# Optimization experiments

Hardware: AMD Instinct MI355X
Metric: run time of the kernel (lower is better)

## Reference

```python
import jax, jax.numpy as jnp
import numpy as np

B, H, L, TAU, THETA = 8192, 256, 4, 8, 8


def setup_inputs() -> dict:
    key = jax.random.key(0)
    ks = jax.random.split(key, 16)
    w = lambda k, shape: (jax.random.normal(k, shape, jnp.float32) * 0.02)
    return {
        "x": jax.random.normal(ks[0], (B, H), jnp.float32),
        "t_att": jax.random.normal(ks[1], (L, TAU, B, H), jnp.float32),
        "s_att": jax.random.normal(ks[2], (L, TAU, B, H), jnp.float32),
        "embed_w": w(ks[3], (H, H)),
        "embed_b": jnp.zeros((H,), jnp.float32),
        "wtn": w(ks[4], (L, H, H)),
        "btn": jnp.zeros((L, H), jnp.float32),
        "wsn": w(ks[5], (L, H, H)),
        "bsn": jnp.zeros((L, H), jnp.float32),
        "wt": w(ks[6], (L, 3 * H, H)),
        "bt": jnp.zeros((L, 3 * H), jnp.float32),
        "ws": w(ks[7], (L, 3 * H, H)),
        "bs": jnp.zeros((L, 3 * H), jnp.float32),
        "out_w": w(ks[8], (H, H)),
        "out_b": jnp.zeros((H,), jnp.float32),
    }


def _forward(x, t_att, s_att, embed_w, embed_b, wtn, btn, wsn, bsn, wt, bt, ws, bs, out_w, out_b):
    n_layers, tau = t_att.shape[0], t_att.shape[1]
    b, h = x.shape
    scale = 1.0 / np.sqrt(h).astype(np.float32)
    theta = THETA

    S = x @ embed_w.T + embed_b  # embed: [B, H]
    # rolling spatial buffers, start as theta zero entries
    t_sp = jnp.zeros((theta, b, h), x.dtype)
    s_sp = jnp.zeros((theta, b, h), x.dtype)

    for i in range(n_layers):
        T_last = t_att[i, -1]  # [B, H]
        # append current S_t / last T_t to spatial buffers, keep last theta
        s_sp = jnp.concatenate([s_sp[1:], S[None]], axis=0)
        t_sp = jnp.concatenate([t_sp[1:], T_last[None]], axis=0)
        # s_att[i].append(S_t); slice last tau -> keys include current S
        s_keys = jnp.concatenate([s_att[i, 1:], S[None]], axis=0)  # [tau, B, H]
        t_vals = t_att[i]  # [tau, B, H]

        s_next = S @ wsn[i].T + bsn[i]
        t_next = T_last @ wtn[i].T + btn[i]

        # temporal attention over last-tau history
        w_t = jax.nn.softmax(jnp.einsum('kbh,bh->kb', s_keys, s_next) * scale, axis=0)
        T_trend = jnp.einsum('kb,kbh->bh', w_t, t_vals)
        t_gate = jax.nn.sigmoid(t_next)
        T_fusion = T_last * t_gate + (1.0 - t_gate) * T_trend

        # spatial attention over last-theta buffer
        w_s = jax.nn.softmax(jnp.einsum('kbh,bh->kb', t_sp, t_next) * scale, axis=0)
        S_trend = jnp.einsum('kb,kbh->bh', w_s, s_sp)
        s_gate = jax.nn.sigmoid(s_next)
        S_fusion = S * s_gate + (1.0 - s_gate) * S_trend

        Tc = T_fusion @ wt[i].T + bt[i]  # [B, 3H]
        Sc = S_fusion @ ws[i].T + bs[i]
        t_g, t_t_, t_s_ = jnp.split(Tc, 3, axis=-1)
        s_g, s_t_, s_s_ = jnp.split(Sc, 3, axis=-1)
        Tg = jax.nn.sigmoid(t_g)
        Sg = jax.nn.sigmoid(s_g)
        # T_new feeds the (stateful) history; S carries to next layer
        S = Sg * s_s_ + (1.0 - Sg) * t_s_

    return jnp.tanh(S @ out_w.T + out_b)


def reference(x, t_att, s_att, embed_w, embed_b, wtn, btn, wsn, bsn, wt, bt, ws, bs, out_w, out_b):
    return _forward(x, t_att, s_att, embed_w, embed_b, wtn, btn, wsn, bsn, wt, bt, ws, bs, out_w, out_b)
```

## Files before the change

kernel.cpp:

```cpp
#include <hip/hip_runtime.h>
#include <cmath>

typedef __attribute__((ext_vector_type(8))) short short8;
typedef __attribute__((ext_vector_type(4))) float f32x4;
typedef __attribute__((ext_vector_type(4))) unsigned short us4;
typedef unsigned short u16;

#define BATCH 8192
#define HDIM  256
static constexpr size_t BH = (size_t)BATCH * HDIM;
#define PAD 264

__device__ __forceinline__ u16 f2bf(float f) {
    union { float f; unsigned u; } v; v.f = f;
    unsigned r = v.u + 0x7FFFu + ((v.u >> 16) & 1u);
    return (u16)(r >> 16);
}
__device__ __forceinline__ float bf2f(u16 u) {
    union { unsigned u; float f; } v; v.u = ((unsigned)u) << 16;
    return v.f;
}
__device__ __forceinline__ float sigmoidf_(float x) {
    return 1.f / (1.f + __expf(-x));
}
__device__ __forceinline__ short8 cvt8(const float* p) {
    f32x4 lo = *(const f32x4*)p, hi = *(const f32x4*)(p + 4);
    short8 t;
    t[0] = (short)f2bf(lo[0]); t[1] = (short)f2bf(lo[1]);
    t[2] = (short)f2bf(lo[2]); t[3] = (short)f2bf(lo[3]);
    t[4] = (short)f2bf(hi[0]); t[5] = (short)f2bf(hi[1]);
    t[6] = (short)f2bf(hi[2]); t[7] = (short)f2bf(hi[3]);
    return t;
}
__device__ __forceinline__ float dot4(const f32x4& a, const float* b) {
    return a[0] * b[0] + a[1] * b[1] + a[2] * b[2] + a[3] * b[3];
}
template<int N>
__device__ __forceinline__ void vmwait() {
    asm volatile("s_waitcnt vmcnt(%0)" :: "n"(N) : "memory");
    __builtin_amdgcn_sched_barrier(0);
}

__global__ __launch_bounds__(256) void convert_weights(
    const float* __restrict__ embed_w, const float* __restrict__ wtn,
    const float* __restrict__ wsn, const float* __restrict__ wt,
    const float* __restrict__ ws, const float* __restrict__ out_w,
    u16* __restrict__ dst)
{
    int idx = blockIdx.x * 256 + threadIdx.x;
    int e = idx * 4;
    if (e >= 22 * 65536) return;
    int c = e >> 16, o = e & 65535;
    const float* src;
    if (c == 0)      src = embed_w + o;
    else if (c < 5)  src = wtn + (size_t)(c - 1) * 65536 + o;
    else if (c < 9)  src = wsn + (size_t)(c - 5) * 65536 + o;
    else if (c < 13) src = wt + (size_t)(c - 9) * 768 * 256 + 512 * 256 + o;
    else if (c < 17) src = ws + (size_t)(c - 13) * 768 * 256 + o;
    else if (c < 21) src = ws + (size_t)(c - 17) * 768 * 256 + 512 * 256 + o;
    else             src = out_w + o;
    f32x4 v = *(const f32x4*)src;
    us4 r;
#pragma unroll
    for (int j = 0; j < 4; ++j) r[j] = f2bf(v[j]);
    *(us4*)(dst + e) = r;
}

template<int I>
__device__ __forceinline__ void issue_row(f32x4 (&buf)[18],
    const float* __restrict__ t_att, const float* __restrict__ s_att,
    int row, int lane)
{
    const size_t ro = (size_t)row * 256 + lane * 4;
    const float* sa = s_att + (size_t)I * 8 * BH + ro;
    const float* ta = t_att + (size_t)I * 8 * BH + ro;
#pragma unroll
    for (int kk = 0; kk < 7; ++kk)
        asm volatile("global_load_dwordx4 %0, %1, off"
                     : "=v"(buf[kk]) : "v"(sa + (size_t)(kk + 1) * BH));
#pragma unroll
    for (int kk = 0; kk < 8; ++kk)
        asm volatile("global_load_dwordx4 %0, %1, off"
                     : "=v"(buf[7 + kk]) : "v"(ta + (size_t)kk * BH));
#pragma unroll
    for (int jj = 0; jj < I; ++jj)
        asm volatile("global_load_dwordx4 %0, %1, off"
                     : "=v"(buf[15 + jj]) : "v"(t_att + ((size_t)jj * 8 + 7) * BH + ro));
}

template<int I>
__device__ __forceinline__ void compute_row(
    const f32x4 (&buf)[18], int rr, int lane,
    u16 (&S_lds)[5][16][PAD], u16 (&sn_lds)[16][PAD], u16 (&tn_lds)[16][PAD],
    u16 (&tf_lds)[16][PAD], u16 (&sf_lds)[16][PAD])
{
    const float scale = 0.0625f;
    us4 snu = *(const us4*)&sn_lds[rr][lane * 4];
    us4 tnu = *(const us4*)&tn_lds[rr][lane * 4];
    us4 scu = *(const us4*)&S_lds[I][rr][lane * 4];
    float sn[4], tn[4], Sc[4];
#pragma unroll
    for (int j = 0; j < 4; ++j) { sn[j] = bf2f(snu[j]); tn[j] = bf2f(tnu[j]); Sc[j] = bf2f(scu[j]); }

    constexpr int NV = 9 + I;
    float v[NV];
#pragma unroll
    for (int kk = 0; kk < 7; ++kk) v[kk] = dot4(buf[kk], sn);
    v[7] = Sc[0] * sn[0] + Sc[1] * sn[1] + Sc[2] * sn[2] + Sc[3] * sn[3];
#pragma unroll
    for (int jj = 0; jj < I; ++jj) v[8 + jj] = dot4(buf[15 + jj], tn);
    v[8 + I] = dot4(buf[14], tn);

#pragma unroll
    for (int o = 32; o > 0; o >>= 1)
#pragma unroll
        for (int u = 0; u < NV; ++u) v[u] += __shfl_xor(v[u], o);

    float m = v[0] * scale;
#pragma unroll
    for (int kk = 1; kk < 8; ++kk) m = fmaxf(m, v[kk] * scale);
    float w8[8], den = 0.f;
#pragma unroll
    for (int kk = 0; kk < 8; ++kk) { w8[kk] = __expf(v[kk] * scale - m); den += w8[kk]; }
    float inv = 1.f / den;

    float Tt[4] = {0.f, 0.f, 0.f, 0.f};
#pragma unroll
    for (int kk = 0; kk < 8; ++kk)
#pragma unroll
        for (int j = 0; j < 4; ++j) Tt[j] += w8[kk] * buf[7 + kk][j];
    us4 ot;
#pragma unroll
    for (int j = 0; j < 4; ++j) {
        float g = sigmoidf_(tn[j]);
        ot[j] = f2bf(buf[14][j] * g + (1.f - g) * Tt[j] * inv);
    }
    *(us4*)&tf_lds[rr][lane * 4] = ot;

    float ms = fmaxf(0.f, v[8 + I] * scale);
#pragma unroll
    for (int jj = 0; jj < I; ++jj) ms = fmaxf(ms, v[8 + jj] * scale);
    float dens = (float)(7 - I) * __expf(-ms);
    float St[4];
    {
        float w = __expf(v[8 + I] * scale - ms);
        dens += w;
#pragma unroll
        for (int j = 0; j < 4; ++j) St[j] = w * Sc[j];
    }
#pragma unroll
    for (int jj = 0; jj < I; ++jj) {
        float w = __expf(v[8 + jj] * scale - ms);
        dens += w;
        us4 shu = *(const us4*)&S_lds[jj][rr][lane * 4];
#pragma unroll
        for (int j = 0; j < 4; ++j) St[j] += w * bf2f(shu[j]);
    }
    float invs = 1.f / dens;
    us4 os;
#pragma unroll
    for (int j = 0; j < 4; ++j) {
        float g = sigmoidf_(sn[j]);
        os[j] = f2bf(Sc[j] * g + (1.f - g) * St[j] * invs);
    }
    *(us4*)&sf_lds[rr][lane * 4] = os;
}

template<int I>
__device__ __forceinline__ void layer_body(
    const float* __restrict__ t_att, const float* __restrict__ s_att,
    const u16* __restrict__ Wbf,
    const float* __restrict__ btn, const float* __restrict__ bsn,
    const float* __restrict__ bt, const float* __restrict__ bs,
    u16 (&S_lds)[5][16][PAD], u16 (&sn_lds)[16][PAD], u16 (&tn_lds)[16][PAD],
    u16 (&tf_lds)[16][PAD], u16 (&sf_lds)[16][PAD],
    int lane, int wave, int lr, int kg, int row0)
{
    {
        const int g = wave >> 1;
        const int n0 = (wave & 1) * 128;
        const u16* Wm = Wbf + (size_t)((g ? 1 : 5) + I) * 65536;
        const float* bias = (g ? btn : bsn) + I * 256;
        f32x4 acc[8] = {};
        for (int k0 = 0; k0 < 256; k0 += 32) {
            int k = k0 + kg * 8;
            short8 a;
            if (g == 0) a = *(const short8*)(&S_lds[I][lr][k]);
            else        a = cvt8(t_att + ((size_t)I * 8 + 7) * BH + (size_t)(row0 + lr) * 256 + k);
#pragma unroll
            for (int nf = 0; nf < 8; ++nf) {
                short8 b = *(const short8*)(Wm + (size_t)(n0 + nf * 16 + lr) * 256 + k);
                acc[nf] = __builtin_amdgcn_mfma_f32_16x16x32_bf16(a, b, acc[nf], 0, 0, 0);
            }
        }
        u16 (*dst)[PAD] = g ? tn_lds : sn_lds;
#pragma unroll
        for (int nf = 0; nf < 8; ++nf) {
            int n = n0 + nf * 16 + lr;
            float bn = bias[n];
#pragma unroll
            for (int r = 0; r < 4; ++r)
                dst[kg * 4 + r][n] = f2bf(acc[nf][r] + bn);
        }
    }
    __syncthreads();

    {
        constexpr int NL = 15 + I;
        const int r0 = wave * 4;
        f32x4 A[18], B[18];
        issue_row<I>(A, t_att, s_att, row0 + r0, lane);
        issue_row<I>(B, t_att, s_att, row0 + r0 + 1, lane);
        vmwait<NL>();
        compute_row<I>(A, r0, lane, S_lds, sn_lds, tn_lds, tf_lds, sf_lds);
        issue_row<I>(A, t_att, s_att, row0 + r0 + 2, lane);
        vmwait<NL>();
        compute_row<I>(B, r0 + 1, lane, S_lds, sn_lds, tn_lds, tf_lds, sf_lds);
        issue_row<I>(B, t_att, s_att, row0 + r0 + 3, lane);
        vmwait<NL>();
        compute_row<I>(A, r0 + 2, lane, S_lds, sn_lds, tn_lds, tf_lds, sf_lds);
        vmwait<0>();
        compute_row<I>(B, r0 + 3, lane, S_lds, sn_lds, tn_lds, tf_lds, sf_lds);
    }
    __syncthreads();

    {
        const int n0 = wave * 64;
        const u16* Wt3 = Wbf + (size_t)(9  + I) * 65536;
        const u16* Ws1 = Wbf + (size_t)(13 + I) * 65536;
        const u16* Ws3 = Wbf + (size_t)(17 + I) * 65536;
        f32x4 aT[4] = {}, aG[4] = {}, aS[4] = {};
        for (int k0 = 0; k0 < 256; k0 += 32) {
            int k = k0 + kg * 8;
            short8 at = *(const short8*)(&tf_lds[lr][k]);
            short8 as = *(const short8*)(&sf_lds[lr][k]);
#pragma unroll
            for (int nf = 0; nf < 4; ++nf) {
                size_t wo = (size_t)(n0 + nf * 16 + lr) * 256 + k;
                aT[nf] = __builtin_amdgcn_mfma_f32_16x16x32_bf16(at, *(const short8*)(Wt3 + wo), aT[nf], 0, 0, 0);
                aG[nf] = __builtin_amdgcn_mfma_f32_16x16x32_bf16(as, *(const short8*)(Ws1 + wo), aG[nf], 0, 0, 0);
                aS[nf] = __builtin_amdgcn_mfma_f32_16x16x32_bf16(as, *(const short8*)(Ws3 + wo), aS[nf], 0, 0, 0);
            }
        }
        const float* b1 = bt + I * 768 + 512;
        const float* b2 = bs + I * 768;
        const float* b3 = bs + I * 768 + 512;
#pragma unroll
        for (int nf = 0; nf < 4; ++nf) {
            int n = n0 + nf * 16 + lr;
            float bb1 = b1[n], bb2 = b2[n], bb3 = b3[n];
#pragma unroll
            for (int r = 0; r < 4; ++r) {
                float gv = sigmoidf_(aG[nf][r] + bb2);
                float vv = gv * (aS[nf][r] + bb3) + (1.f - gv) * (aT[nf][r] + bb1);
                S_lds[I + 1][kg * 4 + r][n] = f2bf(vv);
            }
        }
    }
    __syncthreads();
}

__global__ __launch_bounds__(256, 2) void stau_mega(
    const float* __restrict__ x,
    const float* __restrict__ t_att, const float* __restrict__ s_att,
    const u16* __restrict__ Wbf,
    const float* __restrict__ embed_b,
    const float* __restrict__ btn, const float* __restrict__ bsn,
    const float* __restrict__ bt, const float* __restrict__ bs,
    const float* __restrict__ out_b,
    float* __restrict__ outp)
{
    __shared__ __align__(16) u16 S_lds[5][16][PAD];
    __shared__ __align__(16) u16 sn_lds[16][PAD];
    __shared__ __align__(16) u16 tn_lds[16][PAD];
    __shared__ __align__(16) u16 tf_lds[16][PAD];
    __shared__ __align__(16) u16 sf_lds[16][PAD];

    const int lane = threadIdx.x & 63;
    const int wave = threadIdx.x >> 6;
    const int lr = lane & 15;
    const int kg = lane >> 4;
    const int row0 = blockIdx.x * 16;

    {
        const int n0 = wave * 64;
        f32x4 acc[4] = {};
        for (int k0 = 0; k0 < 256; k0 += 32) {
            int k = k0 + kg * 8;
            short8 a = cvt8(x + (size_t)(row0 + lr) * 256 + k);
#pragma unroll
            for (int nf = 0; nf < 4; ++nf) {
                short8 b = *(const short8*)(Wbf + (size_t)(n0 + nf * 16 + lr) * 256 + k);
                acc[nf] = __builtin_amdgcn_mfma_f32_16x16x32_bf16(a, b, acc[nf], 0, 0, 0);
            }
        }
#pragma unroll
        for (int nf = 0; nf < 4; ++nf) {
            int n = n0 + nf * 16 + lr;
            float bn = embed_b[n];
#pragma unroll
            for (int r = 0; r < 4; ++r)
                S_lds[0][kg * 4 + r][n] = f2bf(acc[nf][r] + bn);
        }
    }
    __syncthreads();

    layer_body<0>(t_att, s_att, Wbf, btn, bsn, bt, bs,
                  S_lds, sn_lds, tn_lds, tf_lds, sf_lds, lane, wave, lr, kg, row0);
    layer_body<1>(t_att, s_att, Wbf, btn, bsn, bt, bs,
                  S_lds, sn_lds, tn_lds, tf_lds, sf_lds, lane, wave, lr, kg, row0);
    layer_body<2>(t_att, s_att, Wbf, btn, bsn, bt, bs,
                  S_lds, sn_lds, tn_lds, tf_lds, sf_lds, lane, wave, lr, kg, row0);
    layer_body<3>(t_att, s_att, Wbf, btn, bsn, bt, bs,
                  S_lds, sn_lds, tn_lds, tf_lds, sf_lds, lane, wave, lr, kg, row0);

    {
        const int n0 = wave * 64;
        const u16* Wo = Wbf + (size_t)21 * 65536;
        f32x4 acc[4] = {};
        for (int k0 = 0; k0 < 256; k0 += 32) {
            int k = k0 + kg * 8;
            short8 a = *(const short8*)(&S_lds[4][lr][k]);
#pragma unroll
            for (int nf = 0; nf < 4; ++nf) {
                short8 b = *(const short8*)(Wo + (size_t)(n0 + nf * 16 + lr) * 256 + k);
                acc[nf] = __builtin_amdgcn_mfma_f32_16x16x32_bf16(a, b, acc[nf], 0, 0, 0);
            }
        }
#pragma unroll
        for (int nf = 0; nf < 4; ++nf) {
            int n = n0 + nf * 16 + lr;
            float bn = out_b[n];
#pragma unroll
            for (int r = 0; r < 4; ++r)
                outp[(size_t)(row0 + kg * 4 + r) * 256 + n] = tanhf(acc[nf][r] + bn);
        }
    }
}

extern "C" void kernel_launch(void* const* d_in, const int* in_sizes, int n_in,
                              void* d_out, int out_size, void* d_ws, size_t ws_size,
                              hipStream_t stream)
{
    (void)in_sizes; (void)n_in; (void)out_size; (void)ws_size;
    const float* x       = (const float*)d_in[0];
    const float* t_att   = (const float*)d_in[1];
    const float* s_att   = (const float*)d_in[2];
    const float* embed_w = (const float*)d_in[3];
    const float* embed_b = (const float*)d_in[4];
    const float* wtn     = (const float*)d_in[5];
    const float* btn     = (const float*)d_in[6];
    const float* wsn     = (const float*)d_in[7];
    const float* bsn     = (const float*)d_in[8];
    const float* wt      = (const float*)d_in[9];
    const float* bt      = (const float*)d_in[10];
    const float* ws_in   = (const float*)d_in[11];
    const float* bs      = (const float*)d_in[12];
    const float* out_w   = (const float*)d_in[13];
    const float* out_b   = (const float*)d_in[14];

    u16* Wbf = (u16*)d_ws;

    convert_weights<<<1408, 256, 0, stream>>>(embed_w, wtn, wsn, wt, ws_in, out_w, Wbf);

    stau_mega<<<BATCH / 16, 256, 0, stream>>>(
        x, t_att, s_att, Wbf, embed_b, btn, bsn, bt, bs, out_b, (float*)d_out);
}
```

Before: 271.9 us.

## Move S history from LDS to global workspace and restructure per-row attention loads

```diff
diff --git a/kernel.cpp b/kernel.cpp
--- a/kernel.cpp
+++ b/kernel.cpp
@@ -9,7 +9,7 @@
 #define BATCH 8192
 #define HDIM  256
 static constexpr size_t BH = (size_t)BATCH * HDIM;
-#define PAD 264
+#define LPAD 264
 
 __device__ __forceinline__ u16 f2bf(float f) {
     union { float f; unsigned u; } v; v.f = f;
@@ -67,49 +67,65 @@
 }
 
 template<int I>
-__device__ __forceinline__ void issue_row(f32x4 (&buf)[18],
+__device__ __forceinline__ void attn_row(
     const float* __restrict__ t_att, const float* __restrict__ s_att,
-    int row, int lane)
-{
-    const size_t ro = (size_t)row * 256 + lane * 4;
+    const u16* __restrict__ S_hist,
+    int brow, int rr, int lane,
+    u16 (&sn_lds)[16][LPAD], u16 (&tn_lds)[16][LPAD],
+    u16 (&tf_lds)[16][LPAD], u16 (&sf_lds)[16][LPAD])
+{
+    const float scale = 0.0625f;
+    const size_t ro = (size_t)brow * 256 + lane * 4;
     const float* sa = s_att + (size_t)I * 8 * BH + ro;
     const float* ta = t_att + (size_t)I * 8 * BH + ro;
+
+    us4 scu;
+    us4 shu[I > 0 ? I : 1];
+    asm volatile("global_load_dwordx2 %0, %1, off"
+                 : "=v"(scu) : "v"(S_hist + (size_t)I * BH + ro));
+#pragma unroll
+    for (int jj = 0; jj < I; ++jj)
+        asm volatile("global_load_dwordx2 %0, %1, off"
+                     : "=v"(shu[jj]) : "v"(S_hist + (size_t)jj * BH + ro));
+
+    f32x4 dbuf[8 + I];
 #pragma unroll
     for (int kk = 0; kk < 7; ++kk)
         asm volatile("global_load_dwordx4 %0, %1, off"
-                     : "=v"(buf[kk]) : "v"(sa + (size_t)(kk + 1) * BH));
-#pragma unroll
-    for (int kk = 0; kk < 8; ++kk)
-        asm volatile("global_load_dwordx4 %0, %1, off"
-                     : "=v"(buf[7 + kk]) : "v"(ta + (size_t)kk * BH));
+                     : "=v"(dbuf[kk]) : "v"(sa + (size_t)(kk + 1) * BH));
 #pragma unroll
     for (int jj = 0; jj < I; ++jj)
         asm volatile("global_load_dwordx4 %0, %1, off"
-                     : "=v"(buf[15 + jj]) : "v"(t_att + ((size_t)jj * 8 + 7) * BH + ro));
-}
-
-template<int I>
-__device__ __forceinline__ void compute_row(
-    const f32x4 (&buf)[18], int rr, int lane,
-    u16 (&S_lds)[5][16][PAD], u16 (&sn_lds)[16][PAD], u16 (&tn_lds)[16][PAD],
-    u16 (&tf_lds)[16][PAD], u16 (&sf_lds)[16][PAD])
-{
-    const float scale = 0.0625f;
+                     : "=v"(dbuf[7 + jj]) : "v"(t_att + ((size_t)jj * 8 + 7) * BH + ro));
+    asm volatile("global_load_dwordx4 %0, %1, off"
+                 : "=v"(dbuf[7 + I]) : "v"(ta + (size_t)7 * BH));
+
+    f32x4 tbuf[7];
+#pragma unroll
+    for (int kk = 0; kk < 7; ++kk)
+        asm volatile("global_load_dwordx4 %0, %1, off"
+                     : "=v"(tbuf[kk]) : "v"(ta + (size_t)kk * BH));
+
     us4 snu = *(const us4*)&sn_lds[rr][lane * 4];
     us4 tnu = *(const us4*)&tn_lds[rr][lane * 4];
-    us4 scu = *(const us4*)&S_lds[I][rr][lane * 4];
-    float sn[4], tn[4], Sc[4];
-#pragma unroll
-    for (int j = 0; j < 4; ++j) { sn[j] = bf2f(snu[j]); tn[j] = bf2f(tnu[j]); Sc[j] = bf2f(scu[j]); }
+    float sn[4], tn[4];
+#pragma unroll
+    for (int j = 0; j < 4; ++j) { sn[j] = bf2f(snu[j]); tn[j] = bf2f(tnu[j]); }
+
+    vmwait<7>();
+
+    float Sc[4];
+#pragma unroll
+    for (int j = 0; j < 4; ++j) Sc[j] = bf2f(scu[j]);
 
     constexpr int NV = 9 + I;
     float v[NV];
 #pragma unroll
-    for (int kk = 0; kk < 7; ++kk) v[kk] = dot4(buf[kk], sn);
+    for (int kk = 0; kk < 7; ++kk) v[kk] = dot4(dbuf[kk], sn);
     v[7] = Sc[0] * sn[0] + Sc[1] * sn[1] + Sc[2] * sn[2] + Sc[3] * sn[3];
 #pragma unroll
-    for (int jj = 0; jj < I; ++jj) v[8 + jj] = dot4(buf[15 + jj], tn);
-    v[8 + I] = dot4(buf[14], tn);
+    for (int jj = 0; jj < I; ++jj) v[8 + jj] = dot4(dbuf[7 + jj], tn);
+    v[8 + I] = dot4(dbuf[7 + I], tn);
 
 #pragma unroll
     for (int o = 32; o > 0; o >>= 1)
@@ -124,16 +140,20 @@
     for (int kk = 0; kk < 8; ++kk) { w8[kk] = __expf(v[kk] * scale - m); den += w8[kk]; }
     float inv = 1.f / den;
 
-    float Tt[4] = {0.f, 0.f, 0.f, 0.f};
-#pragma unroll
-    for (int kk = 0; kk < 8; ++kk)
-#pragma unroll
-        for (int j = 0; j < 4; ++j) Tt[j] += w8[kk] * buf[7 + kk][j];
+    vmwait<0>();
+
+    float Tt[4];
+#pragma unroll
+    for (int j = 0; j < 4; ++j) Tt[j] = w8[7] * dbuf[7 + I][j];
+#pragma unroll
+    for (int kk = 0; kk < 7; ++kk)
+#pragma unroll
+        for (int j = 0; j < 4; ++j) Tt[j] += w8[kk] * tbuf[kk][j];
     us4 ot;
 #pragma unroll
     for (int j = 0; j < 4; ++j) {
         float g = sigmoidf_(tn[j]);
-        ot[j] = f2bf(buf[14][j] * g + (1.f - g) * Tt[j] * inv);
+        ot[j] = f2bf(dbuf[7 + I][j] * g + (1.f - g) * Tt[j] * inv);
     }
     *(us4*)&tf_lds[rr][lane * 4] = ot;
 
@@ -152,9 +172,8 @@
     for (int jj = 0; jj < I; ++jj) {
         float w = __expf(v[8 + jj] * scale - ms);
         dens += w;
-        us4 shu = *(const us4*)&S_lds[jj][rr][lane * 4];
-#pragma unroll
-        for (int j = 0; j < 4; ++j) St[j] += w * bf2f(shu[j]);
+#pragma unroll
+        for (int j = 0; j < 4; ++j) St[j] += w * bf2f(shu[jj][j]);
     }
     float invs = 1.f / dens;
     us4 os;
@@ -169,11 +188,11 @@
 template<int I>
 __device__ __forceinline__ void layer_body(
     const float* __restrict__ t_att, const float* __restrict__ s_att,
-    const u16* __restrict__ Wbf,
+    u16* __restrict__ S_hist, const u16* __restrict__ Wbf,
     const float* __restrict__ btn, const float* __restrict__ bsn,
     const float* __restrict__ bt, const float* __restrict__ bs,
-    u16 (&S_lds)[5][16][PAD], u16 (&sn_lds)[16][PAD], u16 (&tn_lds)[16][PAD],
-    u16 (&tf_lds)[16][PAD], u16 (&sf_lds)[16][PAD],
+    u16 (&sn_lds)[16][LPAD], u16 (&tn_lds)[16][LPAD],
+    u16 (&tf_lds)[16][LPAD], u16 (&sf_lds)[16][LPAD],
     int lane, int wave, int lr, int kg, int row0)
 {
     {
@@ -185,7 +204,7 @@
         for (int k0 = 0; k0 < 256; k0 += 32) {
             int k = k0 + kg * 8;
             short8 a;
-            if (g == 0) a = *(const short8*)(&S_lds[I][lr][k]);
+            if (g == 0) a = *(const short8*)(S_hist + (size_t)I * BH + (size_t)(row0 + lr) * 256 + k);
             else        a = cvt8(t_att + ((size_t)I * 8 + 7) * BH + (size_t)(row0 + lr) * 256 + k);
 #pragma unroll
             for (int nf = 0; nf < 8; ++nf) {
@@ -193,7 +212,7 @@
                 acc[nf] = __builtin_amdgcn_mfma_f32_16x16x32_bf16(a, b, acc[nf], 0, 0, 0);
             }
         }
-        u16 (*dst)[PAD] = g ? tn_lds : sn_lds;
+        u16 (*dst)[LPAD] = g ? tn_lds : sn_lds;
 #pragma unroll
         for (int nf = 0; nf < 8; ++nf) {
             int n = n0 + nf * 16 + lr;
@@ -205,22 +224,11 @@
     }
     __syncthreads();
 
-    {
-        constexpr int NL = 15 + I;
-        const int r0 = wave * 4;
-        f32x4 A[18], B[18];
-        issue_row<I>(A, t_att, s_att, row0 + r0, lane);
-        issue_row<I>(B, t_att, s_att, row0 + r0 + 1, lane);
-        vmwait<NL>();
-        compute_row<I>(A, r0, lane, S_lds, sn_lds, tn_lds, tf_lds, sf_lds);
-        issue_row<I>(A, t_att, s_att, row0 + r0 + 2, lane);
-        vmwait<NL>();
-        compute_row<I>(B, r0 + 1, lane, S_lds, sn_lds, tn_lds, tf_lds, sf_lds);
-        issue_row<I>(B, t_att, s_att, row0 + r0 + 3, lane);
-        vmwait<NL>();
-        compute_row<I>(A, r0 + 2, lane, S_lds, sn_lds, tn_lds, tf_lds, sf_lds);
-        vmwait<0>();
-        compute_row<I>(B, r0 + 3, lane, S_lds, sn_lds, tn_lds, tf_lds, sf_lds);
+#pragma unroll 1
+    for (int q = 0; q < 4; ++q) {
+        int rr = wave * 4 + q;
+        attn_row<I>(t_att, s_att, S_hist, row0 + rr, rr, lane,
+                    sn_lds, tn_lds, tf_lds, sf_lds);
     }
     __syncthreads();
 
@@ -242,6 +250,7 @@
                 aS[nf] = __builtin_amdgcn_mfma_f32_16x16x32_bf16(as, *(const short8*)(Ws3 + wo), aS[nf], 0, 0, 0);
             }
         }
+        u16* Sout = S_hist + (size_t)(I + 1) * BH;
         const float* b1 = bt + I * 768 + 512;
         const float* b2 = bs + I * 768;
         const float* b3 = bs + I * 768 + 512;
@@ -253,7 +262,7 @@
             for (int r = 0; r < 4; ++r) {
                 float gv = sigmoidf_(aG[nf][r] + bb2);
                 float vv = gv * (aS[nf][r] + bb3) + (1.f - gv) * (aT[nf][r] + bb1);
-                S_lds[I + 1][kg * 4 + r][n] = f2bf(vv);
+                Sout[(size_t)(row0 + kg * 4 + r) * 256 + n] = f2bf(vv);
             }
         }
     }
@@ -263,18 +272,17 @@
 __global__ __launch_bounds__(256, 2) void stau_mega(
     const float* __restrict__ x,
     const float* __restrict__ t_att, const float* __restrict__ s_att,
-    const u16* __restrict__ Wbf,
+    u16* __restrict__ S_hist, const u16* __restrict__ Wbf,
     const float* __restrict__ embed_b,
     const float* __restrict__ btn, const float* __restrict__ bsn,
     const float* __restrict__ bt, const float* __restrict__ bs,
     const float* __restrict__ out_b,
     float* __restrict__ outp)
 {
-    __shared__ __align__(16) u16 S_lds[5][16][PAD];
-    __shared__ __align__(16) u16 sn_lds[16][PAD];
-    __shared__ __align__(16) u16 tn_lds[16][PAD];
-    __shared__ __align__(16) u16 tf_lds[16][PAD];
-    __shared__ __align__(16) u16 sf_lds[16][PAD];
+    __shared__ __align__(16) u16 sn_lds[16][LPAD];
+    __shared__ __align__(16) u16 tn_lds[16][LPAD];
+    __shared__ __align__(16) u16 tf_lds[16][LPAD];
+    __shared__ __align__(16) u16 sf_lds[16][LPAD];
 
     const int lane = threadIdx.x & 63;
     const int wave = threadIdx.x >> 6;
@@ -300,27 +308,28 @@
             float bn = embed_b[n];
 #pragma unroll
             for (int r = 0; r < 4; ++r)
-                S_lds[0][kg * 4 + r][n] = f2bf(acc[nf][r] + bn);
+                S_hist[(size_t)(row0 + kg * 4 + r) * 256 + n] = f2bf(acc[nf][r] + bn);
         }
     }
     __syncthreads();
 
-    layer_body<0>(t_att, s_att, Wbf, btn, bsn, bt, bs,
-                  S_lds, sn_lds, tn_lds, tf_lds, sf_lds, lane, wave, lr, kg, row0);
-    layer_body<1>(t_att, s_att, Wbf, btn, bsn, bt, bs,
-                  S_lds, sn_lds, tn_lds, tf_lds, sf_lds, lane, wave, lr, kg, row0);
-    layer_body<2>(t_att, s_att, Wbf, btn, bsn, bt, bs,
-                  S_lds, sn_lds, tn_lds, tf_lds, sf_lds, lane, wave, lr, kg, row0);
-    layer_body<3>(t_att, s_att, Wbf, btn, bsn, bt, bs,
-                  S_lds, sn_lds, tn_lds, tf_lds, sf_lds, lane, wave, lr, kg, row0);
+    layer_body<0>(t_att, s_att, S_hist, Wbf, btn, bsn, bt, bs,
+                  sn_lds, tn_lds, tf_lds, sf_lds, lane, wave, lr, kg, row0);
+    layer_body<1>(t_att, s_att, S_hist, Wbf, btn, bsn, bt, bs,
+                  sn_lds, tn_lds, tf_lds, sf_lds, lane, wave, lr, kg, row0);
+    layer_body<2>(t_att, s_att, S_hist, Wbf, btn, bsn, bt, bs,
+                  sn_lds, tn_lds, tf_lds, sf_lds, lane, wave, lr, kg, row0);
+    layer_body<3>(t_att, s_att, S_hist, Wbf, btn, bsn, bt, bs,
+                  sn_lds, tn_lds, tf_lds, sf_lds, lane, wave, lr, kg, row0);
 
     {
         const int n0 = wave * 64;
         const u16* Wo = Wbf + (size_t)21 * 65536;
+        const u16* S4 = S_hist + (size_t)4 * BH;
         f32x4 acc[4] = {};
         for (int k0 = 0; k0 < 256; k0 += 32) {
             int k = k0 + kg * 8;
-            short8 a = *(const short8*)(&S_lds[4][lr][k]);
+            short8 a = *(const short8*)(S4 + (size_t)(row0 + lr) * 256 + k);
 #pragma unroll
             for (int nf = 0; nf < 4; ++nf) {
                 short8 b = *(const short8*)(Wo + (size_t)(n0 + nf * 16 + lr) * 256 + k);
@@ -359,10 +368,12 @@
     const float* out_w   = (const float*)d_in[13];
     const float* out_b   = (const float*)d_in[14];
 
-    u16* Wbf = (u16*)d_ws;
+    u16* wsp    = (u16*)d_ws;
+    u16* Wbf    = wsp;
+    u16* S_hist = wsp + (size_t)22 * 65536;
 
     convert_weights<<<1408, 256, 0, stream>>>(embed_w, wtn, wsn, wt, ws_in, out_w, Wbf);
 
     stau_mega<<<BATCH / 16, 256, 0, stream>>>(
-        x, t_att, s_att, Wbf, embed_b, btn, bsn, bt, bs, out_b, (float*)d_out);
-}
+        x, t_att, s_att, S_hist, Wbf, embed_b, btn, bsn, bt, bs, out_b, (float*)d_out);
+}
```

Measured after the change: 312.8 us. 1.15x slower.
